# Kernel optimization log

Measured on AMD Instinct MI355X. Metric: run time of the kernel, lower is better.

Reference implementation:

```python
import jax, jax.numpy as jnp
import numpy as np

E, D, DIM, H, DH, MLP = 8, 6, 512, 8, 64, 512
P, S, NC, B = 4, 32, 10, 128
PD = 3 * P * P          # patch_dim = 48
GRID = S // P           # 8
N = GRID * GRID + 1     # 65 tokens (64 patches + cls)


def setup_inputs() -> dict:
    key = jax.random.key(0)
    ks = iter(jax.random.split(key, 16))
    r = lambda *s: jax.random.normal(next(ks), s, jnp.float32) * 0.02
    z = lambda *s: jnp.zeros(s, jnp.float32)
    o = lambda *s: jnp.ones(s, jnp.float32)
    return dict(
        x=jax.random.normal(next(ks), (B, 3, S, S), jnp.float32),
        gate_w=r(E, 3 * S * S), gate_b=z(E),
        pln1_g=o(E, PD), pln1_b=z(E, PD),
        patch_w=r(E, PD, DIM), patch_b=z(E, DIM),
        pln2_g=o(E, DIM), pln2_b=z(E, DIM),
        cls_tok=r(E, DIM), pos_emb=r(E, N, DIM),
        aln_g=o(E, D, DIM), aln_b=z(E, D, DIM),
        qkv_w=r(E, D, DIM, 3 * H * DH),
        out_w=r(E, D, H * DH, DIM), out_b=z(E, D, DIM),
        fln_g=o(E, D, DIM), fln_b=z(E, D, DIM),
        ff1_w=r(E, D, DIM, MLP), ff1_b=z(E, D, MLP),
        ff2_w=r(E, D, MLP, DIM), ff2_b=z(E, D, DIM),
        final_g=o(E, DIM), final_b=z(E, DIM),
        head_w=r(E, DIM, NC), head_b=z(E, NC))


def _ln(x, g, b):
    m = x.mean(-1, keepdims=True)
    v = ((x - m) ** 2).mean(-1, keepdims=True)
    return (x - m) * jax.lax.rsqrt(v + 1e-5) * g + b


LAYER_KEYS = ('aln_g', 'aln_b', 'qkv_w', 'out_w', 'out_b',
              'fln_g', 'fln_b', 'ff1_w', 'ff1_b', 'ff2_w', 'ff2_b')


def _vit(x, p):
    # x: [B, 3, S, S]; p: per-expert param dict (no leading expert axis)
    Bx = x.shape[0]
    # rearrange 'b c (h p1) (w p2) -> b (h w) (p1 p2 c)'
    t = x.reshape(Bx, 3, GRID, P, GRID, P).transpose(0, 2, 4, 3, 5, 1)
    t = t.reshape(Bx, GRID * GRID, PD)
    t = _ln(t, p['pln1_g'], p['pln1_b'])
    t = t @ p['patch_w'] + p['patch_b']
    t = _ln(t, p['pln2_g'], p['pln2_b'])
    cls = jnp.broadcast_to(p['cls_tok'][None, None, :], (Bx, 1, DIM))
    t = jnp.concatenate([cls, t], axis=1) + p['pos_emb'][None]  # [B, N, DIM]

    def block(t, lp):
        g = _ln(t, lp['aln_g'], lp['aln_b'])
        qkv = g @ lp['qkv_w']                       # [B, N, 3*H*DH]
        q, k, v = jnp.split(qkv, 3, axis=-1)
        q = q.reshape(Bx, N, H, DH).transpose(0, 2, 1, 3)
        k = k.reshape(Bx, N, H, DH).transpose(0, 2, 1, 3)
        v = v.reshape(Bx, N, H, DH).transpose(0, 2, 1, 3)
        att = jax.nn.softmax(jnp.einsum('bhid,bhjd->bhij', q, k) * (DH ** -0.5), axis=-1)
        o = jnp.einsum('bhij,bhjd->bhid', att, v).transpose(0, 2, 1, 3).reshape(Bx, N, H * DH)
        t = t + o @ lp['out_w'] + lp['out_b']
        g = _ln(t, lp['fln_g'], lp['fln_b'])
        f = jax.nn.gelu(g @ lp['ff1_w'] + lp['ff1_b'], approximate=False) @ lp['ff2_w'] + lp['ff2_b']
        return t + f, None

    layer_p = {k: p[k] for k in LAYER_KEYS}  # each [D, ...]
    t, _ = jax.lax.scan(block, t, layer_p)
    t = _ln(t, p['final_g'], p['final_b'])
    return t[:, 0] @ p['head_w'] + p['head_b']   # [B, NC]


def _moe(x, params):
    Bx = x.shape[0]
    logits = x.reshape(Bx, -1) @ params['gate_w'].T + params['gate_b']  # [B, E]
    top1 = jnp.argmax(logits, axis=1)                                   # [B]
    expert_p = {k: v for k, v in params.items() if k not in ('gate_w', 'gate_b')}
    all_out = jax.vmap(lambda pp: _vit(x, pp))(expert_p)                # [E, B, NC]
    return all_out[top1, jnp.arange(Bx)]                                # [B, NC]


def reference(x, gate_w, gate_b, pln1_g, pln1_b, patch_w, patch_b, pln2_g, pln2_b,
              cls_tok, pos_emb, aln_g, aln_b, qkv_w, out_w, out_b,
              fln_g, fln_b, ff1_w, ff1_b, ff2_w, ff2_b, final_g, final_b,
              head_w, head_b):
    params = {k: v for k, v in locals().items() if k != 'x'}
    return _moe(x, params)
```

## Files before the change

### kernel.cpp

```cpp
#include <hip/hip_runtime.h>
#include <math.h>

#define EXPERTS 8
#define DEPTH 6
#define DIM 512
#define HEADS 8
#define NCLS 10
#define BATCH 128
#define PD 48
#define NTOK 65
#define NRT256 40
#define NROWSP (NRT256 * 256)

typedef __attribute__((ext_vector_type(4))) float f32x4;
typedef __attribute__((ext_vector_type(8))) __bf16 bf16x8;
typedef unsigned short u16;

#define GLOAD_LDS16(gp, lp)                                                     \
    __builtin_amdgcn_global_load_lds(                                           \
        (const __attribute__((address_space(1))) void*)(gp),                    \
        (__attribute__((address_space(3))) void*)(lp), 16, 0, 0)

__device__ inline u16 f2bf(float f) {
    union { float f; unsigned u; } v; v.f = f;
    unsigned r = v.u + 0x7FFFu + ((v.u >> 16) & 1u);
    return (u16)(r >> 16);
}

__global__ __launch_bounds__(256) void gate_k(const float* __restrict__ x,
                                              const float* __restrict__ gw,
                                              const float* __restrict__ gb,
                                              int* __restrict__ top1) {
    int b = blockIdx.x, tid = threadIdx.x;
    const float* xb = x + (size_t)b * 3072;
    float acc[EXPERTS];
#pragma unroll
    for (int e = 0; e < EXPERTS; ++e) acc[e] = 0.f;
    for (int i = tid; i < 3072; i += 256) {
        float xv = xb[i];
#pragma unroll
        for (int e = 0; e < EXPERTS; ++e)
            acc[e] = fmaf(xv, gw[(size_t)e * 3072 + i], acc[e]);
    }
    __shared__ float red[256];
    __shared__ float logits[EXPERTS];
    for (int e = 0; e < EXPERTS; ++e) {
        red[tid] = acc[e];
        __syncthreads();
        for (int s = 128; s > 0; s >>= 1) {
            if (tid < s) red[tid] += red[tid + s];
            __syncthreads();
        }
        if (tid == 0) logits[e] = red[0] + gb[e];
        __syncthreads();
    }
    if (tid == 0) {
        int best = 0;
        float bv = logits[0];
        for (int e = 1; e < EXPERTS; ++e)
            if (logits[e] > bv) { bv = logits[e]; best = e; }
        top1[b] = best;
    }
}

__global__ __launch_bounds__(128) void route3_k(const int* __restrict__ top1,
                                                int* __restrict__ prow,
                                                int* __restrict__ tile_e) {
    __shared__ int t1[BATCH];
    int tid = threadIdx.x;
    t1[tid] = top1[tid];
    __syncthreads();
    if (tid != 0) return;
    int row = 0, tile = 0;
    for (int e = 0; e < EXPERTS; ++e) {
        int ne = 0;
        for (int b = 0; b < BATCH; ++b)
            if (t1[b] == e) { prow[b] = row + ne * 65; ne++; }
        if (!ne) continue;
        int nt = (ne * 65 + 255) >> 8;
        for (int tt = 0; tt < nt; ++tt) tile_e[tile++] = e;
        row += nt << 8;
    }
    for (; tile < NRT256; ++tile) tile_e[tile] = -1;
}

__global__ __launch_bounds__(256) void patch_k(const float* __restrict__ x,
                                               const float* __restrict__ pln1_g,
                                               const float* __restrict__ pln1_b,
                                               const float* __restrict__ patch_w,
                                               const float* __restrict__ patch_b,
                                               const float* __restrict__ pln2_g,
                                               const float* __restrict__ pln2_b,
                                               const float* __restrict__ cls_tok,
                                               const float* __restrict__ pos_emb,
                                               const int* __restrict__ top1,
                                               const int* __restrict__ prow,
                                               float* __restrict__ t) {
    int n = blockIdx.x, b = blockIdx.y, tid = threadIdx.x;
    int e = top1[b];
    float* trow = t + ((size_t)prow[b] + n) * DIM;
    const float* pe = pos_emb + ((size_t)e * NTOK + n) * DIM;

    if (n == 0) {
        for (int d = tid; d < DIM; d += 256)
            trow[d] = cls_tok[e * DIM + d] + pe[d];
        return;
    }
    int pi = n - 1, h = pi >> 3, w = pi & 7;
    __shared__ float pv[PD];
    __shared__ float red[256];
    if (tid < PD) {
        int p1 = tid / 12, rem = tid % 12, p2 = rem / 3, c = rem % 3;
        pv[tid] = x[((size_t)b * 3 + c) * 1024 + (h * 4 + p1) * 32 + (w * 4 + p2)];
    }
    __syncthreads();
    float m = 0.f, q = 0.f;
    for (int j = 0; j < PD; ++j) { float v = pv[j]; m += v; q += v * v; }
    m *= (1.f / PD);
    q = q * (1.f / PD) - m * m;
    float rs = rsqrtf(q + 1e-5f);
    __syncthreads();
    if (tid < PD)
        pv[tid] = (pv[tid] - m) * rs * pln1_g[e * PD + tid] + pln1_b[e * PD + tid];
    __syncthreads();

    float acc0 = patch_b[e * DIM + tid];
    float acc1 = patch_b[e * DIM + tid + 256];
    for (int j = 0; j < PD; ++j) {
        float v = pv[j];
        const float* wr = patch_w + ((size_t)e * PD + j) * DIM;
        acc0 = fmaf(v, wr[tid], acc0);
        acc1 = fmaf(v, wr[tid + 256], acc1);
    }
    red[tid] = acc0 + acc1;
    __syncthreads();
    for (int s = 128; s > 0; s >>= 1) {
        if (tid < s) red[tid] += red[tid + s];
        __syncthreads();
    }
    float S = red[0];
    __syncthreads();
    red[tid] = acc0 * acc0 + acc1 * acc1;
    __syncthreads();
    for (int s = 128; s > 0; s >>= 1) {
        if (tid < s) red[tid] += red[tid + s];
        __syncthreads();
    }
    float Q = red[0];
    float mean = S * (1.f / DIM);
    float var = Q * (1.f / DIM) - mean * mean;
    float rs2 = rsqrtf(var + 1e-5f);
    trow[tid]       = (acc0 - mean) * rs2 * pln2_g[e * DIM + tid]       + pln2_b[e * DIM + tid]       + pe[tid];
    trow[tid + 256] = (acc1 - mean) * rs2 * pln2_g[e * DIM + tid + 256] + pln2_b[e * DIM + tid + 256] + pe[tid + 256];
}

__global__ __launch_bounds__(256) void ln2_k(const float* __restrict__ src,
                                             u16* __restrict__ dst,
                                             const float* __restrict__ gbase,
                                             const float* __restrict__ bbase,
                                             const int* __restrict__ tile_e,
                                             int gestride) {
    int row = blockIdx.x * 4 + (threadIdx.x >> 6);
    int lane = threadIdx.x & 63;
    int e = tile_e[row >> 8];
    if (e < 0) return;
    const float* s = src + (size_t)row * 512;
    float4 a = *(const float4*)&s[lane * 4];
    float4 b = *(const float4*)&s[256 + lane * 4];
    float sum = a.x + a.y + a.z + a.w + b.x + b.y + b.z + b.w;
    float sq = a.x * a.x + a.y * a.y + a.z * a.z + a.w * a.w +
               b.x * b.x + b.y * b.y + b.z * b.z + b.w * b.w;
#pragma unroll
    for (int off = 32; off > 0; off >>= 1) {
        sum += __shfl_xor(sum, off);
        sq += __shfl_xor(sq, off);
    }
    float mean = sum * (1.f / DIM);
    float rs = rsqrtf(sq * (1.f / DIM) - mean * mean + 1e-5f);
    const float* g = gbase + (size_t)e * gestride;
    const float* bb = bbase + (size_t)e * gestride;
    float4 g0 = *(const float4*)&g[lane * 4];
    float4 g1 = *(const float4*)&g[256 + lane * 4];
    float4 b0 = *(const float4*)&bb[lane * 4];
    float4 b1 = *(const float4*)&bb[256 + lane * 4];
    int swz = (row & 7) << 3;
    u16 o[4];
    o[0] = f2bf((a.x - mean) * rs * g0.x + b0.x);
    o[1] = f2bf((a.y - mean) * rs * g0.y + b0.y);
    o[2] = f2bf((a.z - mean) * rs * g0.z + b0.z);
    o[3] = f2bf((a.w - mean) * rs * g0.w + b0.w);
    *(int2*)&dst[(size_t)row * 512 + ((lane * 4) ^ swz)] = *(int2*)o;
    o[0] = f2bf((b.x - mean) * rs * g1.x + b1.x);
    o[1] = f2bf((b.y - mean) * rs * g1.y + b1.y);
    o[2] = f2bf((b.z - mean) * rs * g1.z + b1.z);
    o[3] = f2bf((b.w - mean) * rs * g1.w + b1.w);
    *(int2*)&dst[(size_t)row * 512 + ((256 + lane * 4) ^ swz)] = *(int2*)o;
}

__device__ inline void wconv_body(const float* __restrict__ s,
                                  u16* __restrict__ d, int N,
                                  int n0, int k0, int tid) {
    __shared__ float tile[32][33];
    int r = tid >> 5, c = tid & 31;
#pragma unroll
    for (int i = 0; i < 4; ++i)
        tile[r + i * 8][c] = s[(size_t)(k0 + r + i * 8) * N + n0 + c];
    __syncthreads();
#pragma unroll
    for (int i = 0; i < 4; ++i) {
        int n = n0 + r + i * 8;
        d[(size_t)n * 512 + ((k0 + c) ^ ((n & 7) << 3))] = f2bf(tile[c][r + i * 8]);
    }
}

__global__ __launch_bounds__(256) void wconv_k(const float* __restrict__ src,
                                               u16* __restrict__ dst, int N) {
    wconv_body(src + (size_t)blockIdx.z * 512 * N, dst + (size_t)blockIdx.z * 512 * N,
               N, blockIdx.x * 32, blockIdx.y * 32, threadIdx.x);
}

__global__ __launch_bounds__(256) void wconv3_k(const float* __restrict__ s0,
                                                const float* __restrict__ s1,
                                                const float* __restrict__ s2,
                                                u16* __restrict__ d0,
                                                u16* __restrict__ d1,
                                                u16* __restrict__ d2) {
    int z = blockIdx.z, which = z / 48, m = z % 48;
    const float* s = (which == 0) ? s0 : (which == 1) ? s1 : s2;
    u16* d = (which == 0) ? d0 : (which == 1) ? d1 : d2;
    wconv_body(s + (size_t)m * 512 * 512, d + (size_t)m * 512 * 512,
               512, blockIdx.x * 32, blockIdx.y * 32, threadIdx.x);
}

template <int N, int OP, int MW>
__global__ __launch_bounds__(256) void mgemm_k(const u16* __restrict__ A,
                                               const u16* __restrict__ Wtbase,
                                               const float* __restrict__ Bbase,
                                               void* __restrict__ Cptr,
                                               const int* __restrict__ tile_e,
                                               int westride, int bestride) {
    constexpr int M = MW * 32;
    constexpr int CT = N / 128;
    constexpr int MTILES = NROWSP / M;
    constexpr int ALOADS = M / 32;
    constexpr int LOADS = ALOADS + 4;
    int orig = blockIdx.x, nwg = MTILES * CT;
    int q = nwg >> 3, r8 = nwg & 7;
    int xcd = orig & 7, off = orig >> 3;
    int wg = (xcd < r8 ? xcd * (q + 1) : r8 * (q + 1) + (xcd - r8) * q) + off;
    int tile = wg / CT, ct = wg - tile * CT;
    int e = tile_e[(tile * M) >> 8];
    if (e < 0) return;
    int row0 = tile * M, c0 = ct * 128;
    const u16* Wt = Wtbase + (size_t)e * westride;

    int tid = threadIdx.x;
    int lane = tid & 63, w = tid >> 6;
    int rl = lane & 15, kg = lane >> 4;
    int wr = w >> 1, wc = w & 1;

    __shared__ __align__(16) u16 As[2][M * 64];
    __shared__ __align__(16) u16 Bs[2][128 * 64];

    f32x4 acc[MW][4];
#pragma unroll
    for (int mt = 0; mt < MW; ++mt)
#pragma unroll
        for (int nt = 0; nt < 4; ++nt) acc[mt][nt] = (f32x4){0.f, 0.f, 0.f, 0.f};

    const u16* Ag = A + (size_t)(row0 + w * (M / 4) + (lane >> 3)) * 512 + (lane & 7) * 8;
    const u16* Bg = Wt + (size_t)(c0 + w * 32 + (lane >> 3)) * 512 + (lane & 7) * 8;
    int aoff = w * (M / 4) * 64;
    int boff = w * 2048;

    int blk0 = (kg ^ (rl & 7)) * 8;
    int blk1 = ((4 + kg) ^ (rl & 7)) * 8;

#pragma unroll
    for (int i = 0; i < ALOADS; ++i)
        GLOAD_LDS16(Ag + i * 8 * 512, &As[0][aoff + i * 512]);
#pragma unroll
    for (int i = 0; i < 4; ++i)
        GLOAD_LDS16(Bg + i * 8 * 512, &Bs[0][boff + i * 512]);

    for (int it = 0; it < 8; ++it) {
        int cur = it & 1;
        if (it < 7) {
            int kk = (it + 1) * 64;
            int nxt = cur ^ 1;
#pragma unroll
            for (int i = 0; i < ALOADS; ++i)
                GLOAD_LDS16(Ag + kk + i * 8 * 512, &As[nxt][aoff + i * 512]);
#pragma unroll
            for (int i = 0; i < 4; ++i)
                GLOAD_LDS16(Bg + kk + i * 8 * 512, &Bs[nxt][boff + i * 512]);
            asm volatile("s_waitcnt vmcnt(%0)" :: "n"(LOADS) : "memory");
        } else {
            asm volatile("s_waitcnt vmcnt(0)" ::: "memory");
        }
        __builtin_amdgcn_s_barrier();
        asm volatile("" ::: "memory");
#pragma unroll
        for (int ks = 0; ks < 2; ++ks) {
            int blk = ks ? blk1 : blk0;
            bf16x8 av[MW], bv[4];
#pragma unroll
            for (int i = 0; i < MW; ++i)
                av[i] = *(const bf16x8*)&As[cur][(wr * (M / 2) + i * 16 + rl) * 64 + blk];
#pragma unroll
            for (int i = 0; i < 4; ++i)
                bv[i] = *(const bf16x8*)&Bs[cur][(wc * 64 + i * 16 + rl) * 64 + blk];
#pragma unroll
            for (int mt = 0; mt < MW; ++mt)
#pragma unroll
                for (int nt = 0; nt < 4; ++nt)
                    acc[mt][nt] = __builtin_amdgcn_mfma_f32_16x16x32_bf16(
                        av[mt], bv[nt], acc[mt][nt], 0, 0, 0);
        }
        asm volatile("" ::: "memory");
        __builtin_amdgcn_s_barrier();
    }

    int rh = lane >> 4;
#pragma unroll
    for (int mt = 0; mt < MW; ++mt)
#pragma unroll
        for (int nt = 0; nt < 4; ++nt)
#pragma unroll
            for (int rr = 0; rr < 4; ++rr) {
                size_t grow = row0 + wr * (M / 2) + mt * 16 + rh * 4 + rr;
                int c = c0 + wc * 64 + nt * 16 + rl;
                float v = acc[mt][nt][rr];
                if (OP == 0) {
                    ((u16*)Cptr)[grow * N + c] = f2bf(v);
                } else if (OP == 1) {
                    ((float*)Cptr)[grow * 512 + c] += v + Bbase[(size_t)e * bestride + c];
                } else {
                    float vb = v + Bbase[(size_t)e * bestride + c];
                    float gl = vb * 0.5f * (1.f + erff(vb * 0.70710678118f));
                    ((u16*)Cptr)[grow * 512 + (c ^ (((int)grow & 7) << 3))] = f2bf(gl);
                }
            }
}

#define ATT_LDS (23040 / 2 + 8320 / 2 + 12288 / 2)
__global__ __launch_bounds__(320) void attn3_k(const u16* __restrict__ qkv,
                                               u16* __restrict__ o,
                                               const int* __restrict__ prow) {
    int b = blockIdx.x & 127, h = blockIdx.x >> 7, tid = threadIdx.x;
    int pr = prow[b];
    __shared__ __align__(16) u16 smem[ATT_LDS];
    u16* Qs = smem;
    u16* Ks = smem + 80 * 72;
    u16* Ps = smem;
    u16* Vs = smem + 2 * 80 * 72;
    u16* Vt = Vs + 65 * 64;

    const u16* base = qkv + (size_t)pr * 1536 + h * 64;

    for (int idx = tid; idx < 640; idx += 320) {
        int r = idx >> 3, q = idx & 7;
        int4 vq = {0, 0, 0, 0}, vk = {0, 0, 0, 0};
        if (r < NTOK) {
            vq = *(const int4*)&base[(size_t)r * 1536 + q * 8];
            vk = *(const int4*)&base[(size_t)r * 1536 + 512 + q * 8];
        }
        *(int4*)&Qs[r * 72 + q * 8] = vq;
        *(int4*)&Ks[r * 72 + q * 8] = vk;
    }
    for (int idx = tid; idx < 520; idx += 320) {
        int r = idx >> 3, q = idx & 7;
        *(int4*)&Vs[r * 64 + q * 8] = *(const int4*)&base[(size_t)r * 1536 + 1024 + q * 8];
    }
    __syncthreads();

    int lane = tid & 63, mt = tid >> 6;
    int rl = lane & 15, kg = lane >> 4, g = lane >> 4;

    f32x4 acc[5];
#pragma unroll
    for (int nt = 0; nt < 5; ++nt) acc[nt] = (f32x4){0.f, 0.f, 0.f, 0.f};

    {
        bf16x8 av0 = *(const bf16x8*)&Qs[(mt * 16 + rl) * 72 + kg * 8];
        bf16x8 av1 = *(const bf16x8*)&Qs[(mt * 16 + rl) * 72 + 32 + kg * 8];
#pragma unroll
        for (int nt = 0; nt < 5; ++nt) {
            bf16x8 bv0 = *(const bf16x8*)&Ks[(nt * 16 + rl) * 72 + kg * 8];
            bf16x8 bv1 = *(const bf16x8*)&Ks[(nt * 16 + rl) * 72 + 32 + kg * 8];
            acc[nt] = __builtin_amdgcn_mfma_f32_16x16x32_bf16(av0, bv0, acc[nt], 0, 0, 0);
            acc[nt] = __builtin_amdgcn_mfma_f32_16x16x32_bf16(av1, bv1, acc[nt], 0, 0, 0);
        }
    }

    for (int idx = tid; idx < 768; idx += 320) {
        int d = idx & 63, kq = idx >> 6;
        u16 tmp[8];
#pragma unroll
        for (int j = 0; j < 8; ++j) {
            int k = kq * 8 + j;
            tmp[j] = (k < NTOK) ? Vs[k * 64 + d] : (u16)0;
        }
        *(int4*)&Vt[d * 96 + kq * 8] = *(int4*)tmp;
    }

#pragma unroll
    for (int r = 0; r < 4; ++r) {
        float m = -3.0e38f;
#pragma unroll
        for (int nt = 0; nt < 5; ++nt) {
            float s = acc[nt][r] * 0.125f;
            if (nt * 16 + rl >= NTOK) s = -3.0e38f;
            acc[nt][r] = s;
            m = fmaxf(m, s);
        }
        m = fmaxf(m, __shfl_xor(m, 1));
        m = fmaxf(m, __shfl_xor(m, 2));
        m = fmaxf(m, __shfl_xor(m, 4));
        m = fmaxf(m, __shfl_xor(m, 8));
        float sum = 0.f;
#pragma unroll
        for (int nt = 0; nt < 5; ++nt) {
            float p = expf(acc[nt][r] - m);
            acc[nt][r] = p;
            sum += p;
        }
        sum += __shfl_xor(sum, 1);
        sum += __shfl_xor(sum, 2);
        sum += __shfl_xor(sum, 4);
        sum += __shfl_xor(sum, 8);
        float inv = 1.f / sum;
#pragma unroll
        for (int nt = 0; nt < 5; ++nt) acc[nt][r] *= inv;
    }
    __syncthreads();

#pragma unroll
    for (int nt = 0; nt < 5; ++nt)
#pragma unroll
        for (int r = 0; r < 4; ++r)
            Ps[(mt * 16 + g * 4 + r) * 96 + nt * 16 + rl] = f2bf(acc[nt][r]);
    for (int idx = tid; idx < 160; idx += 320) {
        int r = idx >> 1, hf = idx & 1;
        *(int4*)&Ps[r * 96 + 80 + hf * 8] = (int4){0, 0, 0, 0};
    }
    __syncthreads();

#pragma unroll
    for (int dt = 0; dt < 4; ++dt) {
        f32x4 oa = {0.f, 0.f, 0.f, 0.f};
#pragma unroll
        for (int s2 = 0; s2 < 3; ++s2) {
            bf16x8 av = *(const bf16x8*)&Ps[(mt * 16 + rl) * 96 + s2 * 32 + kg * 8];
            bf16x8 bv = *(const bf16x8*)&Vt[(dt * 16 + rl) * 96 + s2 * 32 + kg * 8];
            oa = __builtin_amdgcn_mfma_f32_16x16x32_bf16(av, bv, oa, 0, 0, 0);
        }
#pragma unroll
        for (int r = 0; r < 4; ++r) {
            int row = mt * 16 + g * 4 + r;
            if (row < NTOK) {
                int grow = pr + row;
                int c = h * 64 + dt * 16 + rl;
                o[(size_t)grow * DIM + (c ^ ((grow & 7) << 3))] = f2bf(oa[r]);
            }
        }
    }
}

__global__ __launch_bounds__(64) void final_k(const float* __restrict__ t,
                                              const float* __restrict__ fg,
                                              const float* __restrict__ fb,
                                              const float* __restrict__ hw,
                                              const float* __restrict__ hb,
                                              const int* __restrict__ top1,
                                              const int* __restrict__ prow,
                                              float* __restrict__ out) {
    int b = blockIdx.x, lane = threadIdx.x;
    int e = top1[b];
    const float* row = t + (size_t)prow[b] * DIM;
    float v[8], s = 0.f, q = 0.f;
#pragma unroll
    for (int ii = 0; ii < 8; ++ii) {
        v[ii] = row[ii * 64 + lane];
        s += v[ii];
        q += v[ii] * v[ii];
    }
    for (int off = 32; off > 0; off >>= 1) {
        s += __shfl_xor(s, off);
        q += __shfl_xor(q, off);
    }
    float mean = s * (1.f / DIM);
    float var = q * (1.f / DIM) - mean * mean;
    float rs = rsqrtf(var + 1e-5f);
    float nv[8];
#pragma unroll
    for (int ii = 0; ii < 8; ++ii) {
        int d = ii * 64 + lane;
        nv[ii] = (v[ii] - mean) * rs * fg[e * DIM + d] + fb[e * DIM + d];
    }
    for (int c = 0; c < NCLS; ++c) {
        float p = 0.f;
#pragma unroll
        for (int ii = 0; ii < 8; ++ii) {
            int d = ii * 64 + lane;
            p = fmaf(nv[ii], hw[(size_t)e * DIM * NCLS + d * NCLS + c], p);
        }
        for (int off = 32; off > 0; off >>= 1) p += __shfl_xor(p, off);
        if (lane == 0) out[b * NCLS + c] = p + hb[e * NCLS + c];
    }
}

extern "C" void kernel_launch(void* const* d_in, const int* in_sizes, int n_in,
                              void* d_out, int out_size, void* d_ws, size_t ws_size,
                              hipStream_t stream) {
    const float* x       = (const float*)d_in[0];
    const float* gate_w  = (const float*)d_in[1];
    const float* gate_b  = (const float*)d_in[2];
    const float* pln1_g  = (const float*)d_in[3];
    const float* pln1_b  = (const float*)d_in[4];
    const float* patch_w = (const float*)d_in[5];
    const float* patch_b = (const float*)d_in[6];
    const float* pln2_g  = (const float*)d_in[7];
    const float* pln2_b  = (const float*)d_in[8];
    const float* cls_tok = (const float*)d_in[9];
    const float* pos_emb = (const float*)d_in[10];
    const float* aln_g   = (const float*)d_in[11];
    const float* aln_b   = (const float*)d_in[12];
    const float* qkv_w   = (const float*)d_in[13];
    const float* out_w   = (const float*)d_in[14];
    const float* out_b   = (const float*)d_in[15];
    const float* fln_g   = (const float*)d_in[16];
    const float* fln_b   = (const float*)d_in[17];
    const float* ff1_w   = (const float*)d_in[18];
    const float* ff1_b   = (const float*)d_in[19];
    const float* ff2_w   = (const float*)d_in[20];
    const float* ff2_b   = (const float*)d_in[21];
    const float* final_g = (const float*)d_in[22];
    const float* final_b = (const float*)d_in[23];
    const float* head_w  = (const float*)d_in[24];
    const float* head_b  = (const float*)d_in[25];
    float* out = (float*)d_out;

    int* top1   = (int*)d_ws;
    int* prow   = top1 + 128;
    int* tile_e = prow + 128;
    float* t  = (float*)((char*)d_ws + 4096);
    u16* aln  = (u16*)(t + (size_t)NROWSP * DIM);
    u16* qb16 = aln + (size_t)NROWSP * DIM;
    u16* ao16 = qb16 + (size_t)NROWSP * 1536;
    u16* h16  = ao16 + (size_t)NROWSP * DIM;
    u16* wq_t = h16 + (size_t)NROWSP * DIM;
    u16* wo_t = wq_t + (size_t)48 * 1536 * 512;
    u16* w1_t = wo_t + (size_t)48 * 512 * 512;
    u16* w2_t = w1_t + (size_t)48 * 512 * 512;

    gate_k<<<BATCH, 256, 0, stream>>>(x, gate_w, gate_b, top1);
    route3_k<<<1, 128, 0, stream>>>(top1, prow, tile_e);
    patch_k<<<dim3(NTOK, BATCH), 256, 0, stream>>>(x, pln1_g, pln1_b, patch_w, patch_b,
                                                   pln2_g, pln2_b, cls_tok, pos_emb,
                                                   top1, prow, t);
    wconv_k<<<dim3(48, 16, 48), 256, 0, stream>>>(qkv_w, wq_t, 1536);
    wconv3_k<<<dim3(16, 16, 144), 256, 0, stream>>>(out_w, ff1_w, ff2_w, wo_t, w1_t, w2_t);

    for (int l = 0; l < DEPTH; ++l) {
        ln2_k<<<NROWSP / 4, 256, 0, stream>>>(t, aln, aln_g + l * DIM, aln_b + l * DIM,
                                              tile_e, DEPTH * DIM);
        mgemm_k<1536, 0, 4><<<(NROWSP / 128) * 12, 256, 0, stream>>>(
            aln, wq_t + (size_t)l * 1536 * 512, nullptr, qb16, tile_e,
            DEPTH * 512 * 1536, 0);
        attn3_k<<<HEADS * BATCH, 320, 0, stream>>>(qb16, ao16, prow);
        mgemm_k<512, 1, 2><<<(NROWSP / 64) * 4, 256, 0, stream>>>(
            ao16, wo_t + (size_t)l * 512 * 512, out_b + l * DIM, t, tile_e,
            DEPTH * 512 * 512, DEPTH * DIM);
        ln2_k<<<NROWSP / 4, 256, 0, stream>>>(t, aln, fln_g + l * DIM, fln_b + l * DIM,
                                              tile_e, DEPTH * DIM);
        mgemm_k<512, 2, 2><<<(NROWSP / 64) * 4, 256, 0, stream>>>(
            aln, w1_t + (size_t)l * 512 * 512, ff1_b + l * DIM, h16, tile_e,
            DEPTH * 512 * 512, DEPTH * DIM);
        mgemm_k<512, 1, 2><<<(NROWSP / 64) * 4, 256, 0, stream>>>(
            h16, w2_t + (size_t)l * 512 * 512, ff2_b + l * DIM, t, tile_e,
            DEPTH * 512 * 512, DEPTH * DIM);
    }
    final_k<<<BATCH, 64, 0, stream>>>(t, final_g, final_b, head_w, head_b, top1, prow, out);
}
```

Baseline: 802.0 us.

## Swizzle QKV output and load attention tiles via direct global-to-LDS copies

The QKV GEMM now writes its bf16 output with an XOR swizzle on the column index keyed by row. The attention kernel loads Q, K and V straight into unpadded LDS with global_load_lds instead of staging through registers, and de-swizzles on read so LDS bank conflicts are avoided without padding. It also raises wave priority around the MFMA sections. The intent is to cut load latency and register traffic in attention, at the cost of reading past the valid rows, which is why the QKV buffer gains 16 rows of padding.

```diff
diff --git a/kernel.cpp b/kernel.cpp
--- a/kernel.cpp
+++ b/kernel.cpp
@@ -332,7 +332,7 @@
                 int c = c0 + wc * 64 + nt * 16 + rl;
                 float v = acc[mt][nt][rr];
                 if (OP == 0) {
-                    ((u16*)Cptr)[grow * N + c] = f2bf(v);
+                    ((u16*)Cptr)[grow * N + (c ^ (((int)grow & 7) << 3))] = f2bf(v);
                 } else if (OP == 1) {
                     ((float*)Cptr)[grow * 512 + c] += v + Bbase[(size_t)e * bestride + c];
                 } else {
@@ -343,55 +343,67 @@
             }
 }
 
-#define ATT_LDS (23040 / 2 + 8320 / 2 + 12288 / 2)
-__global__ __launch_bounds__(320) void attn3_k(const u16* __restrict__ qkv,
+#define ATT_LDS (80 * 64 + 80 * 64 + 72 * 64 + 64 * 96)
+__global__ __launch_bounds__(320) void attn4_k(const u16* __restrict__ qkv,
                                                u16* __restrict__ o,
                                                const int* __restrict__ prow) {
     int b = blockIdx.x & 127, h = blockIdx.x >> 7, tid = threadIdx.x;
     int pr = prow[b];
     __shared__ __align__(16) u16 smem[ATT_LDS];
     u16* Qs = smem;
-    u16* Ks = smem + 80 * 72;
+    u16* Ks = smem + 80 * 64;
     u16* Ps = smem;
-    u16* Vs = smem + 2 * 80 * 72;
-    u16* Vt = Vs + 65 * 64;
-
-    const u16* base = qkv + (size_t)pr * 1536 + h * 64;
-
-    for (int idx = tid; idx < 640; idx += 320) {
-        int r = idx >> 3, q = idx & 7;
-        int4 vq = {0, 0, 0, 0}, vk = {0, 0, 0, 0};
-        if (r < NTOK) {
-            vq = *(const int4*)&base[(size_t)r * 1536 + q * 8];
-            vk = *(const int4*)&base[(size_t)r * 1536 + 512 + q * 8];
-        }
-        *(int4*)&Qs[r * 72 + q * 8] = vq;
-        *(int4*)&Ks[r * 72 + q * 8] = vk;
-    }
-    for (int idx = tid; idx < 520; idx += 320) {
-        int r = idx >> 3, q = idx & 7;
-        *(int4*)&Vs[r * 64 + q * 8] = *(const int4*)&base[(size_t)r * 1536 + 1024 + q * 8];
-    }
-    __syncthreads();
-
-    int lane = tid & 63, mt = tid >> 6;
+    u16* Vs = smem + 2 * 80 * 64;
+    u16* Vt = Vs + 72 * 64;
+
+    int lane = tid & 63, w = tid >> 6;
+
+    {
+        const u16* qg = qkv + (size_t)(pr + w * 16 + (lane >> 3)) * 1536 +
+                        h * 64 + (lane & 7) * 8;
+        u16* qd = Qs + w * 16 * 64;
+        GLOAD_LDS16(qg, qd);
+        GLOAD_LDS16(qg + 8 * 1536, qd + 512);
+        const u16* kgp = qg + 512;
+        u16* kd = Ks + w * 16 * 64;
+        GLOAD_LDS16(kgp, kd);
+        GLOAD_LDS16(kgp + 8 * 1536, kd + 512);
+        if (w < 4) {
+            const u16* vg = qg + 1024;
+            u16* vd = Vs + w * 16 * 64;
+            GLOAD_LDS16(vg, vd);
+            GLOAD_LDS16(vg + 8 * 1536, vd + 512);
+        } else {
+            const u16* vg = qkv + (size_t)(pr + 64 + (lane >> 3)) * 1536 +
+                            1024 + h * 64 + (lane & 7) * 8;
+            GLOAD_LDS16(vg, Vs + 64 * 64);
+        }
+    }
+    __syncthreads();
+
+    int mt = w;
     int rl = lane & 15, kg = lane >> 4, g = lane >> 4;
+    int skey = ((pr + rl) & 7) << 3;
+    int blkA = (kg * 8) ^ skey;
+    int blkB = ((4 + kg) * 8) ^ skey;
 
     f32x4 acc[5];
 #pragma unroll
     for (int nt = 0; nt < 5; ++nt) acc[nt] = (f32x4){0.f, 0.f, 0.f, 0.f};
 
+    __builtin_amdgcn_s_setprio(1);
     {
-        bf16x8 av0 = *(const bf16x8*)&Qs[(mt * 16 + rl) * 72 + kg * 8];
-        bf16x8 av1 = *(const bf16x8*)&Qs[(mt * 16 + rl) * 72 + 32 + kg * 8];
+        bf16x8 av0 = *(const bf16x8*)&Qs[(mt * 16 + rl) * 64 + blkA];
+        bf16x8 av1 = *(const bf16x8*)&Qs[(mt * 16 + rl) * 64 + blkB];
 #pragma unroll
         for (int nt = 0; nt < 5; ++nt) {
-            bf16x8 bv0 = *(const bf16x8*)&Ks[(nt * 16 + rl) * 72 + kg * 8];
-            bf16x8 bv1 = *(const bf16x8*)&Ks[(nt * 16 + rl) * 72 + 32 + kg * 8];
+            bf16x8 bv0 = *(const bf16x8*)&Ks[(nt * 16 + rl) * 64 + blkA];
+            bf16x8 bv1 = *(const bf16x8*)&Ks[(nt * 16 + rl) * 64 + blkB];
             acc[nt] = __builtin_amdgcn_mfma_f32_16x16x32_bf16(av0, bv0, acc[nt], 0, 0, 0);
             acc[nt] = __builtin_amdgcn_mfma_f32_16x16x32_bf16(av1, bv1, acc[nt], 0, 0, 0);
         }
     }
+    __builtin_amdgcn_s_setprio(0);
 
     for (int idx = tid; idx < 768; idx += 320) {
         int d = idx & 63, kq = idx >> 6;
@@ -399,7 +411,7 @@
 #pragma unroll
         for (int j = 0; j < 8; ++j) {
             int k = kq * 8 + j;
-            tmp[j] = (k < NTOK) ? Vs[k * 64 + d] : (u16)0;
+            tmp[j] = (k < NTOK) ? Vs[k * 64 + (d ^ (((pr + k) & 7) << 3))] : (u16)0;
         }
         *(int4*)&Vt[d * 96 + kq * 8] = *(int4*)tmp;
     }
@@ -446,6 +458,7 @@
     }
     __syncthreads();
 
+    __builtin_amdgcn_s_setprio(1);
 #pragma unroll
     for (int dt = 0; dt < 4; ++dt) {
         f32x4 oa = {0.f, 0.f, 0.f, 0.f};
@@ -465,6 +478,7 @@
             }
         }
     }
+    __builtin_amdgcn_s_setprio(0);
 }
 
 __global__ __launch_bounds__(64) void final_k(const float* __restrict__ t,
@@ -547,7 +561,7 @@
     float* t  = (float*)((char*)d_ws + 4096);
     u16* aln  = (u16*)(t + (size_t)NROWSP * DIM);
     u16* qb16 = aln + (size_t)NROWSP * DIM;
-    u16* ao16 = qb16 + (size_t)NROWSP * 1536;
+    u16* ao16 = qb16 + (size_t)(NROWSP + 16) * 1536;
     u16* h16  = ao16 + (size_t)NROWSP * DIM;
     u16* wq_t = h16 + (size_t)NROWSP * DIM;
     u16* wo_t = wq_t + (size_t)48 * 1536 * 512;
@@ -568,7 +582,7 @@
         mgemm_k<1536, 0, 4><<<(NROWSP / 128) * 12, 256, 0, stream>>>(
             aln, wq_t + (size_t)l * 1536 * 512, nullptr, qb16, tile_e,
             DEPTH * 512 * 1536, 0);
-        attn3_k<<<HEADS * BATCH, 320, 0, stream>>>(qb16, ao16, prow);
+        attn4_k<<<HEADS * BATCH, 320, 0, stream>>>(qb16, ao16, prow);
         mgemm_k<512, 1, 2><<<(NROWSP / 64) * 4, 256, 0, stream>>>(
             ao16, wo_t + (size_t)l * 512 * 512, out_b + l * DIM, t, tile_e,
             DEPTH * 512 * 512, DEPTH * DIM);
```

Measured after the change: 803.0 us (median of 2 runs). No clear change (+0.1%).
